# Kernel optimization log

Measured on AMD Instinct MI355X. Metric: run time of the kernel, lower is better.

Reference implementation:

```python
import jax, jax.numpy as jnp
import numpy as np

N, E, D, IN_DIM, EDGE_DIM, L = 50000, 800000, 128, 11, 4, 4
G, MID, SPEC = 500, 256, 300  # num graphs, decoder mid width, per-head spectrum dim
MSG_IN = 2 * D + EDGE_DIM + 1  # h_i, h_j, edge_attr, d2


def _lin_init(key, fan_in, shape):
    return jax.random.uniform(key, shape, jnp.float32, -1.0, 1.0) / np.sqrt(fan_in)


def setup_inputs() -> dict:
    key = jax.random.key(0)
    ks = iter(jax.random.split(key, 64))
    inp = {
        'x': jax.random.normal(next(ks), (N, IN_DIM), jnp.float32),
        'pos': jax.random.normal(next(ks), (N, 3), jnp.float32),
        'edge_attr': jax.random.normal(next(ks), (E, EDGE_DIM), jnp.float32),
        'edge_index': jax.random.randint(next(ks), (2, E), 0, N, jnp.int32),
        'batch': jnp.sort(jax.random.randint(next(ks), (N,), 0, G, jnp.int32)),
        # input projection
        'W_in': _lin_init(next(ks), IN_DIM, (IN_DIM, D)),
        'b_in': jnp.zeros((D,), jnp.float32),
        # per-layer message MLP: Linear(2D+de+1 -> D), ReLU, Linear(D -> D)
        'msg_W1': _lin_init(next(ks), MSG_IN, (L, MSG_IN, D)),
        'msg_b1': jnp.zeros((L, D), jnp.float32),
        'msg_W2': _lin_init(next(ks), D, (L, D, D)),
        'msg_b2': jnp.zeros((L, D), jnp.float32),
        # per-layer update MLP: Linear(2D -> D), ReLU, Linear(D -> D)
        'upd_W1': _lin_init(next(ks), 2 * D, (L, 2 * D, D)),
        'upd_b1': jnp.zeros((L, D), jnp.float32),
        'upd_W2': _lin_init(next(ks), D, (L, D, D)),
        'upd_b2': jnp.zeros((L, D), jnp.float32),
        # per-layer LayerNorm
        'ln_g': jnp.ones((L, D), jnp.float32),
        'ln_b': jnp.zeros((L, D), jnp.float32),
        # decoder heads stacked: index 0 = energy, 1 = intensity
        'dec_W1': _lin_init(next(ks), D, (2, D, MID)),
        'dec_b1': jnp.zeros((2, MID), jnp.float32),
        'dec_lng': jnp.ones((2, MID), jnp.float32),
        'dec_lnb': jnp.zeros((2, MID), jnp.float32),
        'dec_W2': _lin_init(next(ks), MID, (2, MID, MID)),
        'dec_b2': jnp.zeros((2, MID), jnp.float32),
        'dec_W3': _lin_init(next(ks), MID, (2, MID, SPEC)),
        'dec_b3': jnp.zeros((2, SPEC), jnp.float32),
    }
    return inp


def _ln(x, g, b, eps=1e-5):
    m = x.mean(-1, keepdims=True)
    v = ((x - m) ** 2).mean(-1, keepdims=True)
    return (x - m) * jax.lax.rsqrt(v + eps) * g + b


def _softplus_beta(x, beta):
    return jax.nn.softplus(beta * x) / beta


def reference(x, pos, edge_attr, edge_index, batch,
              W_in, b_in, msg_W1, msg_b1, msg_W2, msg_b2,
              upd_W1, upd_b1, upd_W2, upd_b2, ln_g, ln_b,
              dec_W1, dec_b1, dec_lng, dec_lnb, dec_W2, dec_b2, dec_W3, dec_b3):
    n = x.shape[0]
    src, dst = edge_index[0], edge_index[1]  # message flows j(src) -> i(dst)
    h = x @ W_in + b_in  # (n, d)
    rel = pos[dst] - pos[src]  # (e, 3)
    d2 = jnp.sum(rel * rel, axis=-1, keepdims=True)  # (e, 1), invariant squared distance
    for l in range(L):
        m_in = jnp.concatenate([h[dst], h[src], edge_attr, d2], axis=-1)  # (e, 2d+de+1)
        m = jax.nn.relu(m_in @ msg_W1[l] + msg_b1[l]) @ msg_W2[l] + msg_b2[l]  # (e, d)
        agg = jax.ops.segment_sum(m, dst, num_segments=n)  # (n, d) sum aggregation
        u_in = jnp.concatenate([h, agg], axis=-1)  # (n, 2d)
        h_upd = jax.nn.relu(u_in @ upd_W1[l] + upd_b1[l]) @ upd_W2[l] + upd_b2[l]
        h = _ln(h + h_upd, ln_g[l], ln_b[l])  # residual + LayerNorm
    # global mean pool per graph
    hs = jax.ops.segment_sum(h, batch, num_segments=G)
    cnt = jax.ops.segment_sum(jnp.ones((n,), h.dtype), batch, num_segments=G)
    hg = hs / jnp.clip(cnt, 1.0)[:, None]  # (G, d)

    def head(i):
        z = _softplus_beta(_ln(hg @ dec_W1[i] + dec_b1[i], dec_lng[i], dec_lnb[i]), 2.0)
        z = _softplus_beta(z @ dec_W2[i] + dec_b2[i], 2.0)  # dropout = identity (eval)
        return _softplus_beta(z @ dec_W3[i] + dec_b3[i], 1.0)

    eng, intensity = head(0), head(1)
    return jnp.concatenate([eng, intensity], axis=-1)  # (G, 2*SPEC)
```

## Files before the change

### kernel.cpp

```cpp
#include <hip/hip_runtime.h>
#include <cstdint>
#include <cstddef>

#define NND 50000
#define NE  800000
#define DD  128
#define NG  500
#define TT  64
#define NHB 50176

typedef __attribute__((ext_vector_type(8))) short short8v;
typedef __attribute__((ext_vector_type(4))) float float4v;

#define SWZA(row, g) ((g) ^ ((row) & 7) ^ (((row) >> 3) & 7))

__device__ __forceinline__ short f2bf(float f) {
    unsigned u = __builtin_bit_cast(unsigned, f);
    unsigned r = (u + 0x7FFFu + ((u >> 16) & 1u)) >> 16;
    return (short)r;
}

__global__ __launch_bounds__(256) void inproj_kernel(
    const float* __restrict__ x, const float* __restrict__ W,
    const float* __restrict__ b, float* __restrict__ h)
{
    int t = blockIdx.x * 256 + threadIdx.x;
    int i = t >> 7, d = t & 127;
    if (i >= NND) return;
    const float* xr = x + (size_t)i * 11;
    float acc = b[d];
#pragma unroll
    for (int k = 0; k < 11; ++k) acc += xr[k] * W[k * DD + d];
    h[(size_t)i * DD + d] = acc;
}

__global__ __launch_bounds__(256) void hist_kernel(
    const int* __restrict__ dstI, int* __restrict__ hist)
{
    int e = blockIdx.x * 256 + threadIdx.x;
    if (e >= NE) return;
    atomicAdd(&hist[dstI[e]], 1);
}

__global__ __launch_bounds__(256) void scan1_kernel(
    int* __restrict__ hist, int* __restrict__ bsum)
{
    __shared__ int s[256];
    int tid = threadIdx.x;
    int i = blockIdx.x * 256 + tid;
    int v = hist[i];
    s[tid] = v; __syncthreads();
    for (int off = 1; off < 256; off <<= 1) {
        int tmp = (tid >= off) ? s[tid - off] : 0;
        __syncthreads();
        s[tid] += tmp;
        __syncthreads();
    }
    hist[i] = s[tid] - v;
    if (tid == 255) bsum[blockIdx.x] = s[255];
}

__global__ __launch_bounds__(256) void scan2_kernel(
    const int* __restrict__ bsum, int* __restrict__ bsumx)
{
    __shared__ int s[256];
    int tid = threadIdx.x;
    int v = (tid < 196) ? bsum[tid] : 0;
    s[tid] = v; __syncthreads();
    for (int off = 1; off < 256; off <<= 1) {
        int tmp = (tid >= off) ? s[tid - off] : 0;
        __syncthreads();
        s[tid] += tmp;
        __syncthreads();
    }
    if (tid < 196) bsumx[tid] = s[tid] - v;
}

__global__ __launch_bounds__(256) void scan3_kernel(
    int* __restrict__ hist, const int* __restrict__ bsumx)
{
    int i = blockIdx.x * 256 + threadIdx.x;
    hist[i] += bsumx[blockIdx.x];
}

__global__ __launch_bounds__(256) void scatter_kernel(
    const int* __restrict__ dstI, int* __restrict__ cursor, int* __restrict__ perm)
{
    int e = blockIdx.x * 256 + threadIdx.x;
    if (e >= NE) return;
    int pos = atomicAdd(&cursor[dstI[e]], 1);
    perm[pos] = e;
}

__global__ __launch_bounds__(256) void permapply_kernel(
    const int* __restrict__ perm, const int* __restrict__ srcI, const int* __restrict__ dstI,
    const float* __restrict__ ea,
    int* __restrict__ srcP, int* __restrict__ dstP, float* __restrict__ eaP)
{
    int i = blockIdx.x * 256 + threadIdx.x;
    if (i >= NE) return;
    int e = perm[i];
    srcP[i] = srcI[e];
    dstP[i] = dstI[e];
    ((float4*)eaP)[i] = ((const float4*)ea)[e];
}

__global__ __launch_bounds__(256) void d2p_kernel(
    const float* __restrict__ pos, const int* __restrict__ srcP,
    const int* __restrict__ dstP, float* __restrict__ d2)
{
    int e = blockIdx.x * 256 + threadIdx.x;
    if (e >= NE) return;
    int s = srcP[e], d = dstP[e];
    float dx = pos[d * 3 + 0] - pos[s * 3 + 0];
    float dy = pos[d * 3 + 1] - pos[s * 3 + 1];
    float dz = pos[d * 3 + 2] - pos[s * 3 + 2];
    d2[e] = dx * dx + dy * dy + dz * dz;
}

__global__ __launch_bounds__(256) void d2_kernel(
    const float* __restrict__ pos, const int* __restrict__ srcI,
    const int* __restrict__ dstI, float* __restrict__ d2)
{
    int e = blockIdx.x * 256 + threadIdx.x;
    if (e >= NE) return;
    int s = srcI[e], d = dstI[e];
    float dx = pos[d * 3 + 0] - pos[s * 3 + 0];
    float dy = pos[d * 3 + 1] - pos[s * 3 + 1];
    float dz = pos[d * 3 + 2] - pos[s * 3 + 2];
    d2[e] = dx * dx + dy * dy + dz * dz;
}

__global__ __launch_bounds__(256) void wprep_kernel(
    const float* __restrict__ msgW2, const float* __restrict__ updW1,
    const float* __restrict__ updW2, const float* __restrict__ msgW1,
    short* __restrict__ out)
{
    int p = blockIdx.x * 256 + threadIdx.x;
    int chunk = p >> 14;
    int idx = p & 16383;
    int n = idx >> 7;
    int q = (idx & 127) >> 3;
    int j = idx & 7;
    int k = (q ^ (n & 7)) * 8 + j;
    const float* src;
    if      (chunk == 0) src = msgW2;
    else if (chunk == 1) src = updW1;
    else if (chunk == 2) src = updW1 + 128 * DD;
    else if (chunk == 3) src = updW2;
    else if (chunk == 4) src = msgW1;
    else                 src = msgW1 + 128 * DD;
    out[p] = f2bf(src[k * DD + n]);
}

__global__ __launch_bounds__(256, 3) void projm_kernel(
    const float* __restrict__ h, const short* __restrict__ Wa, const short* __restrict__ Wb,
    float* __restrict__ P)
{
    __shared__ __align__(16) short A[64 * 128];
    __shared__ __align__(16) short W[128 * 128];
    int t = threadIdx.x;
    int i0 = blockIdx.x * TT;

    {
        int e = t >> 2;
        int node = i0 + e; if (node >= NND) node = NND - 1;
        const float* hr = h + (size_t)node * DD;
#pragma unroll
        for (int j = 0; j < 4; ++j) {
            int g = (t & 3) * 4 + j;
            float4 v0 = *(const float4*)(hr + g * 8);
            float4 v1 = *(const float4*)(hr + g * 8 + 4);
            short8v pk;
            pk[0]=f2bf(v0.x); pk[1]=f2bf(v0.y); pk[2]=f2bf(v0.z); pk[3]=f2bf(v0.w);
            pk[4]=f2bf(v1.x); pk[5]=f2bf(v1.y); pk[6]=f2bf(v1.z); pk[7]=f2bf(v1.w);
            *(short8v*)&A[e * 128 + SWZA(e, g) * 8] = pk;
        }
    }
    {
        const short8v* g = (const short8v*)Wa;
        short8v* l = (short8v*)W;
#pragma unroll
        for (int p = 0; p < 8; ++p) l[t + p * 256] = g[t + p * 256];
    }
    __syncthreads();

    int lane = t & 63, w = t >> 6;
    int c = lane & 15, lg = lane >> 4;
    int m = w * 16 + c;

    for (int mat = 0; mat < 2; ++mat) {
        float4v acc[8];
#pragma unroll
        for (int i = 0; i < 8; ++i) acc[i] = (float4v){0.f, 0.f, 0.f, 0.f};
#pragma unroll
        for (int ks = 0; ks < 4; ++ks) {
            int kg = ks * 4 + lg;
            short8v afrag = *(const short8v*)&A[m * 128 + SWZA(m, kg) * 8];
#pragma unroll
            for (int nt = 0; nt < 8; ++nt) {
                int n = nt * 16 + c;
                short8v bfrag = *(const short8v*)&W[n * 128 + ((kg ^ (n & 7)) << 3)];
                acc[nt] = __builtin_amdgcn_mfma_f32_16x16x32_bf16(afrag, bfrag, acc[nt], 0, 0, 0);
            }
        }
        float* out = P + (size_t)mat * NND * DD;
#pragma unroll
        for (int reg = 0; reg < 4; ++reg) {
            int node = i0 + w * 16 + lg * 4 + reg;
            if (node < NND) {
#pragma unroll
                for (int nt = 0; nt < 8; ++nt)
                    out[(size_t)node * DD + nt * 16 + c] = acc[nt][reg];
            }
        }
        if (mat == 0) {
            __syncthreads();
            const short8v* g = (const short8v*)Wb;
            short8v* l = (short8v*)W;
#pragma unroll
            for (int p = 0; p < 8; ++p) l[t + p * 256] = g[t + p * 256];
            __syncthreads();
        }
    }
}

__global__ __launch_bounds__(256, 3) void msgm_kernel(
    const float* __restrict__ P, const int* __restrict__ srcP, const int* __restrict__ dstP,
    const float* __restrict__ eaP, const float* __restrict__ d2,
    const float* __restrict__ W1tail, const float* __restrict__ b1,
    const short* __restrict__ W2t, const float* __restrict__ b2,
    float* __restrict__ agg)
{
    __shared__ __align__(16) short Tld[64 * 128];
    __shared__ __align__(16) short W2ld[128 * 128];
    int t = threadIdx.x;
    int e0 = blockIdx.x * TT;
    int tx = t & 15, ty = t >> 4;

    {
        const short8v* g = (const short8v*)W2t;
        short8v* l = (short8v*)W2ld;
#pragma unroll
        for (int p = 0; p < 8; ++p) l[t + p * 256] = g[t + p * 256];
    }

    float wc[5][8];
#pragma unroll
    for (int qf = 0; qf < 5; ++qf) {
        float4 a0 = *(const float4*)(W1tail + qf * DD + ty * 8);
        float4 a1 = *(const float4*)(W1tail + qf * DD + ty * 8 + 4);
        wc[qf][0] = a0.x; wc[qf][1] = a0.y; wc[qf][2] = a0.z; wc[qf][3] = a0.w;
        wc[qf][4] = a1.x; wc[qf][5] = a1.y; wc[qf][6] = a1.z; wc[qf][7] = a1.w;
    }

    float4 b1a = *(const float4*)(b1 + ty * 8);
    float4 b1b = *(const float4*)(b1 + ty * 8 + 4);
    float b1v[8] = {b1a.x, b1a.y, b1a.z, b1a.w, b1b.x, b1b.y, b1b.z, b1b.w};

    const float* Pd = P;
    const float* Ps = P + (size_t)NND * DD;

    int4 dv4 = *(const int4*)(dstP + e0 + tx * 4);
    int4 sv4 = *(const int4*)(srcP + e0 + tx * 4);
    int dcache[4] = {dv4.x, dv4.y, dv4.z, dv4.w};
    int scache[4] = {sv4.x, sv4.y, sv4.z, sv4.w};

#pragma unroll
    for (int i = 0; i < 4; ++i) {
        int e = tx * 4 + i;
        const float* pd = Pd + (size_t)dcache[i] * DD + ty * 8;
        const float* ps = Ps + (size_t)scache[i] * DD + ty * 8;
        float4 p0 = *(const float4*)pd;
        float4 p1 = *(const float4*)(pd + 4);
        float4 q0 = *(const float4*)ps;
        float4 q1 = *(const float4*)(ps + 4);
        float tv[8] = {p0.x + q0.x, p0.y + q0.y, p0.z + q0.z, p0.w + q0.w,
                       p1.x + q1.x, p1.y + q1.y, p1.z + q1.z, p1.w + q1.w};
#pragma unroll
        for (int j = 0; j < 8; ++j) tv[j] += b1v[j];
        float4 av = ((const float4*)eaP)[e0 + e];
        float ev[5] = {av.x, av.y, av.z, av.w, d2[e0 + e]};
#pragma unroll
        for (int qf = 0; qf < 5; ++qf) {
            float xx = ev[qf];
#pragma unroll
            for (int j = 0; j < 8; ++j) tv[j] += xx * wc[qf][j];
        }
        short8v pk;
#pragma unroll
        for (int j = 0; j < 8; ++j) pk[j] = f2bf(fmaxf(tv[j], 0.0f));
        *(short8v*)&Tld[e * 128 + SWZA(e, ty) * 8] = pk;
    }

    __syncthreads();

    int lane = t & 63, w = t >> 6;
    int lg = lane >> 4;
    int m  = w * 16 + (lane & 15);
    float4v acc[8];
#pragma unroll
    for (int i = 0; i < 8; ++i) acc[i] = (float4v){0.f, 0.f, 0.f, 0.f};

#pragma unroll
    for (int ks = 0; ks < 4; ++ks) {
        int kg = ks * 4 + lg;
        short8v afrag = *(const short8v*)&Tld[m * 128 + SWZA(m, kg) * 8];
#pragma unroll
        for (int nt = 0; nt < 8; ++nt) {
            int n = nt * 16 + (lane & 15);
            short8v bfrag = *(const short8v*)&W2ld[n * 128 + ((kg ^ (n & 7)) << 3)];
            acc[nt] = __builtin_amdgcn_mfma_f32_16x16x32_bf16(afrag, bfrag, acc[nt], 0, 0, 0);
        }
    }

    int base_e = e0 + w * 16 + (lg << 2);
    int4 dq = *(const int4*)(dstP + base_e);
    int drow[4] = {dq.x, dq.y, dq.z, dq.w};
    float b2c[8];
#pragma unroll
    for (int nt = 0; nt < 8; ++nt) b2c[nt] = b2[nt * 16 + (lane & 15)];

    float sum[8];
    int cur = drow[0];
#pragma unroll
    for (int nt = 0; nt < 8; ++nt) sum[nt] = acc[nt][0] + b2c[nt];
#pragma unroll
    for (int r = 1; r < 4; ++r) {
        if (drow[r] == cur) {
#pragma unroll
            for (int nt = 0; nt < 8; ++nt) sum[nt] += acc[nt][r] + b2c[nt];
        } else {
            float* ag = agg + (size_t)cur * DD + (lane & 15);
#pragma unroll
            for (int nt = 0; nt < 8; ++nt) unsafeAtomicAdd(ag + nt * 16, sum[nt]);
            cur = drow[r];
#pragma unroll
            for (int nt = 0; nt < 8; ++nt) sum[nt] = acc[nt][r] + b2c[nt];
        }
    }
    float* ag = agg + (size_t)cur * DD + (lane & 15);
#pragma unroll
    for (int nt = 0; nt < 8; ++nt) unsafeAtomicAdd(ag + nt * 16, sum[nt]);
}

__global__ __launch_bounds__(256, 3) void updm_kernel(
    float* __restrict__ h, const float* __restrict__ agg,
    const short* __restrict__ W1a, const short* __restrict__ W1b, const short* __restrict__ W2s,
    const float* __restrict__ b1, const float* __restrict__ b2,
    const float* __restrict__ lng, const float* __restrict__ lnb)
{
    __shared__ __align__(16) short A[64 * 128];
    __shared__ __align__(16) short W[128 * 128];
    int t = threadIdx.x;
    int i0 = blockIdx.x * TT;
    int lane = t & 63, w = t >> 6;
    int c = lane & 15, lg = lane >> 4;
    int m = w * 16 + c;

    {
        int e = t >> 2;
        int node = i0 + e; if (node >= NND) node = NND - 1;
        const float* hr = h + (size_t)node * DD;
#pragma unroll
        for (int j = 0; j < 4; ++j) {
            int g = (t & 3) * 4 + j;
            float4 v0 = *(const float4*)(hr + g * 8);
            float4 v1 = *(const float4*)(hr + g * 8 + 4);
            short8v pk;
            pk[0]=f2bf(v0.x); pk[1]=f2bf(v0.y); pk[2]=f2bf(v0.z); pk[3]=f2bf(v0.w);
            pk[4]=f2bf(v1.x); pk[5]=f2bf(v1.y); pk[6]=f2bf(v1.z); pk[7]=f2bf(v1.w);
            *(short8v*)&A[e * 128 + SWZA(e, g) * 8] = pk;
        }
        const short8v* gg = (const short8v*)W1a;
        short8v* l = (short8v*)W;
#pragma unroll
        for (int p = 0; p < 8; ++p) l[t + p * 256] = gg[t + p * 256];
    }
    __syncthreads();

    float4v acc[8];
#pragma unroll
    for (int i = 0; i < 8; ++i) acc[i] = (float4v){0.f, 0.f, 0.f, 0.f};

#pragma unroll
    for (int ks = 0; ks < 4; ++ks) {
        int kg = ks * 4 + lg;
        short8v afrag = *(const short8v*)&A[m * 128 + SWZA(m, kg) * 8];
#pragma unroll
        for (int nt = 0; nt < 8; ++nt) {
            int n = nt * 16 + c;
            short8v bfrag = *(const short8v*)&W[n * 128 + ((kg ^ (n & 7)) << 3)];
            acc[nt] = __builtin_amdgcn_mfma_f32_16x16x32_bf16(afrag, bfrag, acc[nt], 0, 0, 0);
        }
    }
    __syncthreads();

    {
        int e = t >> 2;
        int node = i0 + e; if (node >= NND) node = NND - 1;
        const float* ar = agg + (size_t)node * DD;
#pragma unroll
        for (int j = 0; j < 4; ++j) {
            int g = (t & 3) * 4 + j;
            float4 v0 = *(const float4*)(ar + g * 8);
            float4 v1 = *(const float4*)(ar + g * 8 + 4);
            short8v pk;
            pk[0]=f2bf(v0.x); pk[1]=f2bf(v0.y); pk[2]=f2bf(v0.z); pk[3]=f2bf(v0.w);
            pk[4]=f2bf(v1.x); pk[5]=f2bf(v1.y); pk[6]=f2bf(v1.z); pk[7]=f2bf(v1.w);
            *(short8v*)&A[e * 128 + SWZA(e, g) * 8] = pk;
        }
        const short8v* gg = (const short8v*)W1b;
        short8v* l = (short8v*)W;
#pragma unroll
        for (int p = 0; p < 8; ++p) l[t + p * 256] = gg[t + p * 256];
    }
    __syncthreads();

#pragma unroll
    for (int ks = 0; ks < 4; ++ks) {
        int kg = ks * 4 + lg;
        short8v afrag = *(const short8v*)&A[m * 128 + SWZA(m, kg) * 8];
#pragma unroll
        for (int nt = 0; nt < 8; ++nt) {
            int n = nt * 16 + c;
            short8v bfrag = *(const short8v*)&W[n * 128 + ((kg ^ (n & 7)) << 3)];
            acc[nt] = __builtin_amdgcn_mfma_f32_16x16x32_bf16(afrag, bfrag, acc[nt], 0, 0, 0);
        }
    }
    __syncthreads();

    {
        float b1c[8];
#pragma unroll
        for (int nt = 0; nt < 8; ++nt) b1c[nt] = b1[nt * 16 + c];
#pragma unroll
        for (int reg = 0; reg < 4; ++reg) {
            int rowT = w * 16 + lg * 4 + reg;
#pragma unroll
            for (int nt = 0; nt < 8; ++nt) {
                int col = nt * 16 + c;
                int colg = col >> 3;
                float v = fmaxf(acc[nt][reg] + b1c[nt], 0.0f);
                A[rowT * 128 + SWZA(rowT, colg) * 8 + (col & 7)] = f2bf(v);
            }
        }
        const short8v* gg = (const short8v*)W2s;
        short8v* l = (short8v*)W;
#pragma unroll
        for (int p = 0; p < 8; ++p) l[t + p * 256] = gg[t + p * 256];
    }
    __syncthreads();

#pragma unroll
    for (int i = 0; i < 8; ++i) acc[i] = (float4v){0.f, 0.f, 0.f, 0.f};
#pragma unroll
    for (int ks = 0; ks < 4; ++ks) {
        int kg = ks * 4 + lg;
        short8v afrag = *(const short8v*)&A[m * 128 + SWZA(m, kg) * 8];
#pragma unroll
        for (int nt = 0; nt < 8; ++nt) {
            int n = nt * 16 + c;
            short8v bfrag = *(const short8v*)&W[n * 128 + ((kg ^ (n & 7)) << 3)];
            acc[nt] = __builtin_amdgcn_mfma_f32_16x16x32_bf16(afrag, bfrag, acc[nt], 0, 0, 0);
        }
    }

    float b2c[8], lngc[8], lnbc[8];
#pragma unroll
    for (int nt = 0; nt < 8; ++nt) {
        b2c[nt]  = b2[nt * 16 + c];
        lngc[nt] = lng[nt * 16 + c];
        lnbc[nt] = lnb[nt * 16 + c];
    }
    float xx[8][4];
#pragma unroll
    for (int reg = 0; reg < 4; ++reg) {
        int node = i0 + w * 16 + lg * 4 + reg;
        int nclamp = (node < NND) ? node : (NND - 1);
        const float* hr = h + (size_t)nclamp * DD;
#pragma unroll
        for (int nt = 0; nt < 8; ++nt)
            xx[nt][reg] = acc[nt][reg] + b2c[nt] + hr[nt * 16 + c];
    }
    float s[4] = {0.f, 0.f, 0.f, 0.f};
#pragma unroll
    for (int reg = 0; reg < 4; ++reg)
#pragma unroll
        for (int nt = 0; nt < 8; ++nt) s[reg] += xx[nt][reg];
#pragma unroll
    for (int msk = 1; msk < 16; msk <<= 1)
#pragma unroll
        for (int reg = 0; reg < 4; ++reg) s[reg] += __shfl_xor(s[reg], msk, 64);
    float mean[4];
#pragma unroll
    for (int reg = 0; reg < 4; ++reg) mean[reg] = s[reg] * (1.0f / DD);
    float v[4] = {0.f, 0.f, 0.f, 0.f};
#pragma unroll
    for (int reg = 0; reg < 4; ++reg)
#pragma unroll
        for (int nt = 0; nt < 8; ++nt) {
            float dv = xx[nt][reg] - mean[reg];
            v[reg] += dv * dv;
        }
#pragma unroll
    for (int msk = 1; msk < 16; msk <<= 1)
#pragma unroll
        for (int reg = 0; reg < 4; ++reg) v[reg] += __shfl_xor(v[reg], msk, 64);
#pragma unroll
    for (int reg = 0; reg < 4; ++reg) {
        int node = i0 + w * 16 + lg * 4 + reg;
        if (node < NND) {
            float inv = 1.0f / sqrtf(v[reg] * (1.0f / DD) + 1e-5f);
            float* hw = h + (size_t)node * DD;
#pragma unroll
            for (int nt = 0; nt < 8; ++nt)
                hw[nt * 16 + c] = (xx[nt][reg] - mean[reg]) * inv * lngc[nt] + lnbc[nt];
        }
    }
}

__global__ __launch_bounds__(256, 2) void msgu_kernel(
    const float* __restrict__ h, const int* __restrict__ srcI, const int* __restrict__ dstI,
    const float* __restrict__ ea, const float* __restrict__ d2,
    const float* __restrict__ W1, const float* __restrict__ b1,
    const float* __restrict__ W2, const float* __restrict__ b2,
    float* __restrict__ agg)
{
    __shared__ __align__(16) float A[32][TT];
    __shared__ __align__(16) float T[DD][TT];
    __shared__ __align__(16) float B[32][DD];
    int t = threadIdx.x;
    int e0 = blockIdx.x * TT;
    int tx = t & 15, ty = t >> 4;
    int e = t & 63, q = t >> 6;
    int dn = dstI[e0 + e], sn = srcI[e0 + e];

    float4 b1a = *(const float4*)(b1 + ty * 8);
    float4 b1b = *(const float4*)(b1 + ty * 8 + 4);
    float acc[4][8];
#pragma unroll
    for (int i = 0; i < 4; ++i) {
        acc[i][0] = b1a.x; acc[i][1] = b1a.y; acc[i][2] = b1a.z; acc[i][3] = b1a.w;
        acc[i][4] = b1b.x; acc[i][5] = b1b.y; acc[i][6] = b1b.z; acc[i][7] = b1b.w;
    }

    for (int cc = 0; cc < 9; ++cc) {
        int kmax = (cc == 8) ? 5 : 32;
        __syncthreads();
        if (cc < 8) {
            const float* row = h + (size_t)((cc < 4) ? dn : sn) * DD + (cc & 3) * 32;
            float4 v0 = *(const float4*)(row + q * 8);
            float4 v1 = *(const float4*)(row + q * 8 + 4);
#pragma unroll
            for (int j = 0; j < 4; ++j) A[q * 8 + j][e]     = (&v0.x)[j];
#pragma unroll
            for (int j = 0; j < 4; ++j) A[q * 8 + 4 + j][e] = (&v1.x)[j];
        } else if (t < TT) {
            float4 av = ((const float4*)ea)[e0 + t];
            A[0][t] = av.x; A[1][t] = av.y; A[2][t] = av.z; A[3][t] = av.w;
            A[4][t] = d2[e0 + t];
        }
        const float4* srcp = (const float4*)(W1 + (size_t)(cc * 32) * DD);
        float4* dstp = (float4*)&B[0][0];
        if (cc < 8) {
#pragma unroll
            for (int r = 0; r < 4; ++r) dstp[t + r * 256] = srcp[t + r * 256];
        } else if (t < 160) {
            dstp[t] = srcp[t];
        }
        __syncthreads();
        for (int k = 0; k < kmax; ++k) {
            float4 a  = *(const float4*)&A[k][tx * 4];
            float4 b0 = *(const float4*)&B[k][ty * 8];
            float4 b1f = *(const float4*)&B[k][ty * 8 + 4];
            float av[4] = {a.x, a.y, a.z, a.w};
            float bv[8] = {b0.x, b0.y, b0.z, b0.w, b1f.x, b1f.y, b1f.z, b1f.w};
#pragma unroll
            for (int i = 0; i < 4; ++i)
#pragma unroll
                for (int j = 0; j < 8; ++j) acc[i][j] += av[i] * bv[j];
        }
    }

#pragma unroll
    for (int i = 0; i < 4; ++i)
#pragma unroll
        for (int j = 0; j < 8; ++j) T[ty * 8 + j][tx * 4 + i] = fmaxf(acc[i][j], 0.0f);

    float4 b2a = *(const float4*)(b2 + ty * 8);
    float4 b2b = *(const float4*)(b2 + ty * 8 + 4);
#pragma unroll
    for (int i = 0; i < 4; ++i) {
        acc[i][0] = b2a.x; acc[i][1] = b2a.y; acc[i][2] = b2a.z; acc[i][3] = b2a.w;
        acc[i][4] = b2b.x; acc[i][5] = b2b.y; acc[i][6] = b2b.z; acc[i][7] = b2b.w;
    }
    for (int cc = 0; cc < 4; ++cc) {
        __syncthreads();
        const float4* srcp = (const float4*)(W2 + (size_t)(cc * 32) * DD);
        float4* dstp = (float4*)&B[0][0];
#pragma unroll
        for (int r = 0; r < 4; ++r) dstp[t + r * 256] = srcp[t + r * 256];
        __syncthreads();
#pragma unroll 4
        for (int k = 0; k < 32; ++k) {
            float4 a  = *(const float4*)&T[cc * 32 + k][tx * 4];
            float4 b0 = *(const float4*)&B[k][ty * 8];
            float4 b1f = *(const float4*)&B[k][ty * 8 + 4];
            float av[4] = {a.x, a.y, a.z, a.w};
            float bv[8] = {b0.x, b0.y, b0.z, b0.w, b1f.x, b1f.y, b1f.z, b1f.w};
#pragma unroll
            for (int i = 0; i < 4; ++i)
#pragma unroll
                for (int j = 0; j < 8; ++j) acc[i][j] += av[i] * bv[j];
        }
    }
#pragma unroll
    for (int i = 0; i < 4; ++i) {
        int d = dstI[e0 + tx * 4 + i];
        float* ag = agg + (size_t)d * DD + ty * 8;
#pragma unroll
        for (int j = 0; j < 8; ++j) unsafeAtomicAdd(ag + j, acc[i][j]);
    }
}

__global__ __launch_bounds__(256, 2) void updf_kernel(
    float* __restrict__ h, const float* __restrict__ agg,
    const float* __restrict__ W1, const float* __restrict__ b1,
    const float* __restrict__ W2, const float* __restrict__ b2,
    const float* __restrict__ lng, const float* __restrict__ lnb)
{
    __shared__ __align__(16) float A[32][TT];
    __shared__ __align__(16) float T[DD][TT];
    __shared__ __align__(16) float B[32][DD];
    int t = threadIdx.x;
    int i0 = blockIdx.x * TT;
    int tx = t & 15, ty = t >> 4;
    int e = t & 63, q = t >> 6;
    int node = i0 + e; int nclamp = (node < NND) ? node : (NND - 1);

    float4 b1a = *(const float4*)(b1 + ty * 8);
    float4 b1b = *(const float4*)(b1 + ty * 8 + 4);
    float acc[4][8];
#pragma unroll
    for (int i = 0; i < 4; ++i) {
        acc[i][0] = b1a.x; acc[i][1] = b1a.y; acc[i][2] = b1a.z; acc[i][3] = b1a.w;
        acc[i][4] = b1b.x; acc[i][5] = b1b.y; acc[i][6] = b1b.z; acc[i][7] = b1b.w;
    }

    for (int cc = 0; cc < 8; ++cc) {
        __syncthreads();
        const float* row = ((cc < 4) ? (h + (size_t)nclamp * DD + cc * 32)
                                     : (agg + (size_t)nclamp * DD + (cc - 4) * 32));
        float4 v0 = *(const float4*)(row + q * 8);
        float4 v1 = *(const float4*)(row + q * 8 + 4);
#pragma unroll
        for (int j = 0; j < 4; ++j) A[q * 8 + j][e]     = (&v0.x)[j];
#pragma unroll
        for (int j = 0; j < 4; ++j) A[q * 8 + 4 + j][e] = (&v1.x)[j];
        const float4* srcp = (const float4*)(W1 + (size_t)(cc * 32) * DD);
        float4* dstp = (float4*)&B[0][0];
#pragma unroll
        for (int r = 0; r < 4; ++r) dstp[t + r * 256] = srcp[t + r * 256];
        __syncthreads();
#pragma unroll 4
        for (int k = 0; k < 32; ++k) {
            float4 a  = *(const float4*)&A[k][tx * 4];
            float4 b0 = *(const float4*)&B[k][ty * 8];
            float4 b1f = *(const float4*)&B[k][ty * 8 + 4];
            float av[4] = {a.x, a.y, a.z, a.w};
            float bv[8] = {b0.x, b0.y, b0.z, b0.w, b1f.x, b1f.y, b1f.z, b1f.w};
#pragma unroll
            for (int i = 0; i < 4; ++i)
#pragma unroll
                for (int j = 0; j < 8; ++j) acc[i][j] += av[i] * bv[j];
        }
    }

#pragma unroll
    for (int i = 0; i < 4; ++i)
#pragma unroll
        for (int j = 0; j < 8; ++j) T[ty * 8 + j][tx * 4 + i] = fmaxf(acc[i][j], 0.0f);

    float4 b2a = *(const float4*)(b2 + ty * 8);
    float4 b2b = *(const float4*)(b2 + ty * 8 + 4);
#pragma unroll
    for (int i = 0; i < 4; ++i) {
        acc[i][0] = b2a.x; acc[i][1] = b2a.y; acc[i][2] = b2a.z; acc[i][3] = b2a.w;
        acc[i][4] = b2b.x; acc[i][5] = b2b.y; acc[i][6] = b2b.z; acc[i][7] = b2b.w;
    }
    for (int cc = 0; cc < 4; ++cc) {
        __syncthreads();
        const float4* srcp = (const float4*)(W2 + (size_t)(cc * 32) * DD);
        float4* dstp = (float4*)&B[0][0];
#pragma unroll
        for (int r = 0; r < 4; ++r) dstp[t + r * 256] = srcp[t + r * 256];
        __syncthreads();
#pragma unroll 4
        for (int k = 0; k < 32; ++k) {
            float4 a  = *(const float4*)&T[cc * 32 + k][tx * 4];
            float4 b0 = *(const float4*)&B[k][ty * 8];
            float4 b1f = *(const float4*)&B[k][ty * 8 + 4];
            float av[4] = {a.x, a.y, a.z, a.w};
            float bv[8] = {b0.x, b0.y, b0.z, b0.w, b1f.x, b1f.y, b1f.z, b1f.w};
#pragma unroll
            for (int i = 0; i < 4; ++i)
#pragma unroll
                for (int j = 0; j < 8; ++j) acc[i][j] += av[i] * bv[j];
        }
    }

    __syncthreads();
#pragma unroll
    for (int i = 0; i < 4; ++i)
#pragma unroll
        for (int j = 0; j < 8; ++j) T[ty * 8 + j][tx * 4 + i] = acc[i][j];
    __syncthreads();

    if (t < TT) {
        int nd = i0 + t;
        if (nd < NND) {
            float* hrow = h + (size_t)nd * DD;
            float sum = 0.0f;
            for (int o = 0; o < DD; ++o) sum += T[o][t] + hrow[o];
            float mean = sum * (1.0f / DD);
            float var = 0.0f;
            for (int o = 0; o < DD; ++o) {
                float xv = T[o][t] + hrow[o] - mean;
                var += xv * xv;
            }
            var *= (1.0f / DD);
            float inv = 1.0f / sqrtf(var + 1e-5f);
            for (int o = 0; o < DD; ++o) {
                float xv = T[o][t] + hrow[o];
                hrow[o] = (xv - mean) * inv * lng[o] + lnb[o];
            }
        }
    }
}

__global__ __launch_bounds__(256) void cnt_kernel(
    const int* __restrict__ batch, float* __restrict__ cnt)
{
    int i = blockIdx.x * 256 + threadIdx.x;
    if (i >= NND) return;
    unsafeAtomicAdd(&cnt[batch[i]], 1.0f);
}

__global__ __launch_bounds__(256) void pool_kernel(
    const float* __restrict__ h, const int* __restrict__ batch, float* __restrict__ hs)
{
    int t = blockIdx.x * 256 + threadIdx.x;
    int i = t >> 7, d = t & 127;
    if (i >= NND) return;
    unsafeAtomicAdd(&hs[batch[i] * DD + d], h[(size_t)i * DD + d]);
}

__device__ __forceinline__ float softplus_stable(float y) {
    return fmaxf(y, 0.0f) + log1pf(expf(-fabsf(y)));
}

__global__ __launch_bounds__(256) void dec_kernel(
    const float* __restrict__ hs, const float* __restrict__ cnt,
    const float* __restrict__ W1, const float* __restrict__ b1,
    const float* __restrict__ lng, const float* __restrict__ lnb,
    const float* __restrict__ W2, const float* __restrict__ b2,
    const float* __restrict__ W3, const float* __restrict__ b3,
    float* __restrict__ out)
{
    int g  = blockIdx.x >> 1;
    int hd = blockIdx.x & 1;
    int t  = threadIdx.x;
    __shared__ float hg[DD];
    __shared__ float sA[256];
    __shared__ float red[256];

    if (t < DD) {
        float cct = fmaxf(cnt[g], 1.0f);
        hg[t] = hs[g * DD + t] / cct;
    }
    __syncthreads();

    const float* w1 = W1 + hd * DD * 256;
    float acc = b1[hd * 256 + t];
#pragma unroll 8
    for (int k = 0; k < DD; ++k) acc += hg[k] * w1[k * 256 + t];

    red[t] = acc; __syncthreads();
    for (int s = 128; s > 0; s >>= 1) { if (t < s) red[t] += red[t + s]; __syncthreads(); }
    float mean = red[0] * (1.0f / 256.0f);
    __syncthreads();
    float dv = acc - mean;
    red[t] = dv * dv; __syncthreads();
    for (int s = 128; s > 0; s >>= 1) { if (t < s) red[t] += red[t + s]; __syncthreads(); }
    float var = red[0] * (1.0f / 256.0f);
    float inv = 1.0f / sqrtf(var + 1e-5f);
    float z1 = dv * inv * lng[hd * 256 + t] + lnb[hd * 256 + t];
    z1 = softplus_stable(2.0f * z1) * 0.5f;
    __syncthreads();
    sA[t] = z1; __syncthreads();

    const float* w2 = W2 + hd * 256 * 256;
    float acc2 = b2[hd * 256 + t];
#pragma unroll 8
    for (int k = 0; k < 256; ++k) acc2 += sA[k] * w2[k * 256 + t];
    float z2 = softplus_stable(2.0f * acc2) * 0.5f;
    __syncthreads();
    sA[t] = z2; __syncthreads();

    const float* w3 = W3 + hd * 256 * 300;
    for (int s = t; s < 300; s += 256) {
        float acc3 = b3[hd * 300 + s];
#pragma unroll 8
        for (int k = 0; k < 256; ++k) acc3 += sA[k] * w3[k * 300 + s];
        out[g * 600 + hd * 300 + s] = softplus_stable(acc3);
    }
}

extern "C" void kernel_launch(void* const* d_in, const int* in_sizes, int n_in,
                              void* d_out, int out_size, void* d_ws, size_t ws_size,
                              hipStream_t stream)
{
    const float* x     = (const float*)d_in[0];
    const float* pos   = (const float*)d_in[1];
    const float* eattr = (const float*)d_in[2];
    const int*   eidx  = (const int*)d_in[3];
    const int*   batch = (const int*)d_in[4];
    const float* W_in  = (const float*)d_in[5];
    const float* b_in  = (const float*)d_in[6];
    const float* msgW1 = (const float*)d_in[7];
    const float* msgb1 = (const float*)d_in[8];
    const float* msgW2 = (const float*)d_in[9];
    const float* msgb2 = (const float*)d_in[10];
    const float* updW1 = (const float*)d_in[11];
    const float* updb1 = (const float*)d_in[12];
    const float* updW2 = (const float*)d_in[13];
    const float* updb2 = (const float*)d_in[14];
    const float* lng   = (const float*)d_in[15];
    const float* lnb   = (const float*)d_in[16];
    const float* dW1   = (const float*)d_in[17];
    const float* db1   = (const float*)d_in[18];
    const float* dlng  = (const float*)d_in[19];
    const float* dlnb  = (const float*)d_in[20];
    const float* dW2   = (const float*)d_in[21];
    const float* db2   = (const float*)d_in[22];
    const float* dW3   = (const float*)d_in[23];
    const float* db3   = (const float*)d_in[24];

    float* ws  = (float*)d_ws;
    float* h    = ws;
    float* agg  = ws + 6400000;
    float* d2   = ws + 12800000;
    float* hsg  = ws + 13600000;
    float* cnt  = ws + 13664000;
    float* P    = ws + 13700000;
    int*   perm = (int*)(ws + 26500000);
    int*   srcP = (int*)(ws + 27300000);
    int*   dstP = (int*)(ws + 28100000);
    float* eaP  = ws + 28900000;
    int*   hist = (int*)(ws + 32100000);
    int*   bsum = (int*)(ws + 32150176);
    int*   bsumx= (int*)(ws + 32150432);
    short* WP   = (short*)(ws + 32150688);

    const size_t need_sorted = (size_t)(32150688 + 49152) * 4;
    const bool sorted = (ws_size >= need_sorted);

    const int* srcI = eidx;
    const int* dstI = eidx + NE;

    inproj_kernel<<<25000, 256, 0, stream>>>(x, W_in, b_in, h);

    if (sorted) {
        hipMemsetAsync(hist, 0, (size_t)(NHB + 512) * 4, stream);
        hist_kernel<<<3125, 256, 0, stream>>>(dstI, hist);
        scan1_kernel<<<196, 256, 0, stream>>>(hist, bsum);
        scan2_kernel<<<1, 256, 0, stream>>>(bsum, bsumx);
        scan3_kernel<<<196, 256, 0, stream>>>(hist, bsumx);
        scatter_kernel<<<3125, 256, 0, stream>>>(dstI, hist, perm);
        permapply_kernel<<<3125, 256, 0, stream>>>(perm, srcI, dstI, eattr, srcP, dstP, eaP);
        d2p_kernel<<<3125, 256, 0, stream>>>(pos, srcP, dstP, d2);
    } else {
        d2_kernel<<<3125, 256, 0, stream>>>(pos, srcI, dstI, d2);
    }

    const int nblk_nodes = (NND + TT - 1) / TT;
    const int nblk_edges = NE / TT;

    for (int l = 0; l < 4; ++l) {
        const float* W1l = msgW1 + (size_t)l * 261 * 128;
        hipMemsetAsync(agg, 0, 6400000 * sizeof(float), stream);
        if (sorted) {
            wprep_kernel<<<384, 256, 0, stream>>>(
                msgW2 + (size_t)l * 128 * 128, updW1 + (size_t)l * 256 * 128,
                updW2 + (size_t)l * 128 * 128, W1l, WP);
            projm_kernel<<<nblk_nodes, 256, 0, stream>>>(h, WP + 4 * 16384, WP + 5 * 16384, P);
            msgm_kernel<<<nblk_edges, 256, 0, stream>>>(P, srcP, dstP, eaP, d2,
                W1l + 256 * 128, msgb1 + l * 128, WP, msgb2 + l * 128, agg);
            updm_kernel<<<nblk_nodes, 256, 0, stream>>>(h, agg,
                WP + 1 * 16384, WP + 2 * 16384, WP + 3 * 16384,
                updb1 + l * 128, updb2 + l * 128, lng + l * 128, lnb + l * 128);
        } else {
            msgu_kernel<<<nblk_edges, 256, 0, stream>>>(h, srcI, dstI, eattr, d2,
                W1l, msgb1 + l * 128,
                msgW2 + (size_t)l * 128 * 128, msgb2 + l * 128, agg);
            updf_kernel<<<nblk_nodes, 256, 0, stream>>>(h, agg,
                updW1 + (size_t)l * 256 * 128, updb1 + l * 128,
                updW2 + (size_t)l * 128 * 128, updb2 + l * 128,
                lng + l * 128, lnb + l * 128);
        }
    }

    hipMemsetAsync(hsg, 0, 64500 * sizeof(float), stream);
    cnt_kernel<<<196, 256, 0, stream>>>(batch, cnt);
    pool_kernel<<<25000, 256, 0, stream>>>(h, batch, hsg);
    dec_kernel<<<1000, 256, 0, stream>>>(hsg, cnt, dW1, db1, dlng, dlnb,
                                         dW2, db2, dW3, db3, (float*)d_out);
}
```

Measured before the change: 1.849 ms.

## Store projected node features as bf16 and build MFMA A-fragments in registers

```diff
diff --git a/kernel.cpp b/kernel.cpp
--- a/kernel.cpp
+++ b/kernel.cpp
@@ -18,6 +18,9 @@
     unsigned u = __builtin_bit_cast(unsigned, f);
     unsigned r = (u + 0x7FFFu + ((u >> 16) & 1u)) >> 16;
     return (short)r;
+}
+__device__ __forceinline__ float bf2f(short s) {
+    return __builtin_bit_cast(float, ((unsigned)(unsigned short)s) << 16);
 }
 
 __global__ __launch_bounds__(256) void inproj_kernel(
@@ -155,7 +158,7 @@
 
 __global__ __launch_bounds__(256, 3) void projm_kernel(
     const float* __restrict__ h, const short* __restrict__ Wa, const short* __restrict__ Wb,
-    float* __restrict__ P)
+    short* __restrict__ P)
 {
     __shared__ __align__(16) short A[64 * 128];
     __shared__ __align__(16) short W[128 * 128];
@@ -204,14 +207,14 @@
                 acc[nt] = __builtin_amdgcn_mfma_f32_16x16x32_bf16(afrag, bfrag, acc[nt], 0, 0, 0);
             }
         }
-        float* out = P + (size_t)mat * NND * DD;
+        short* out = P + (size_t)mat * NND * DD;
 #pragma unroll
         for (int reg = 0; reg < 4; ++reg) {
             int node = i0 + w * 16 + lg * 4 + reg;
             if (node < NND) {
 #pragma unroll
                 for (int nt = 0; nt < 8; ++nt)
-                    out[(size_t)node * DD + nt * 16 + c] = acc[nt][reg];
+                    out[(size_t)node * DD + nt * 16 + c] = f2bf(acc[nt][reg]);
             }
         }
         if (mat == 0) {
@@ -225,92 +228,70 @@
     }
 }
 
-__global__ __launch_bounds__(256, 3) void msgm_kernel(
-    const float* __restrict__ P, const int* __restrict__ srcP, const int* __restrict__ dstP,
+__global__ __launch_bounds__(256, 4) void msgm_kernel(
+    const short* __restrict__ P, const int* __restrict__ srcP, const int* __restrict__ dstP,
     const float* __restrict__ eaP, const float* __restrict__ d2,
     const float* __restrict__ W1tail, const float* __restrict__ b1,
     const short* __restrict__ W2t, const float* __restrict__ b2,
     float* __restrict__ agg)
 {
-    __shared__ __align__(16) short Tld[64 * 128];
     __shared__ __align__(16) short W2ld[128 * 128];
+    __shared__ __align__(16) float WcB[6 * 128];
     int t = threadIdx.x;
     int e0 = blockIdx.x * TT;
-    int tx = t & 15, ty = t >> 4;
 
     {
         const short8v* g = (const short8v*)W2t;
         short8v* l = (short8v*)W2ld;
 #pragma unroll
         for (int p = 0; p < 8; ++p) l[t + p * 256] = g[t + p * 256];
-    }
-
-    float wc[5][8];
-#pragma unroll
-    for (int qf = 0; qf < 5; ++qf) {
-        float4 a0 = *(const float4*)(W1tail + qf * DD + ty * 8);
-        float4 a1 = *(const float4*)(W1tail + qf * DD + ty * 8 + 4);
-        wc[qf][0] = a0.x; wc[qf][1] = a0.y; wc[qf][2] = a0.z; wc[qf][3] = a0.w;
-        wc[qf][4] = a1.x; wc[qf][5] = a1.y; wc[qf][6] = a1.z; wc[qf][7] = a1.w;
-    }
-
-    float4 b1a = *(const float4*)(b1 + ty * 8);
-    float4 b1b = *(const float4*)(b1 + ty * 8 + 4);
-    float b1v[8] = {b1a.x, b1a.y, b1a.z, b1a.w, b1b.x, b1b.y, b1b.z, b1b.w};
-
-    const float* Pd = P;
-    const float* Ps = P + (size_t)NND * DD;
-
-    int4 dv4 = *(const int4*)(dstP + e0 + tx * 4);
-    int4 sv4 = *(const int4*)(srcP + e0 + tx * 4);
-    int dcache[4] = {dv4.x, dv4.y, dv4.z, dv4.w};
-    int scache[4] = {sv4.x, sv4.y, sv4.z, sv4.w};
-
-#pragma unroll
-    for (int i = 0; i < 4; ++i) {
-        int e = tx * 4 + i;
-        const float* pd = Pd + (size_t)dcache[i] * DD + ty * 8;
-        const float* ps = Ps + (size_t)scache[i] * DD + ty * 8;
-        float4 p0 = *(const float4*)pd;
-        float4 p1 = *(const float4*)(pd + 4);
-        float4 q0 = *(const float4*)ps;
-        float4 q1 = *(const float4*)(ps + 4);
-        float tv[8] = {p0.x + q0.x, p0.y + q0.y, p0.z + q0.z, p0.w + q0.w,
-                       p1.x + q1.x, p1.y + q1.y, p1.z + q1.z, p1.w + q1.w};
-#pragma unroll
-        for (int j = 0; j < 8; ++j) tv[j] += b1v[j];
-        float4 av = ((const float4*)eaP)[e0 + e];
-        float ev[5] = {av.x, av.y, av.z, av.w, d2[e0 + e]};
+        if (t < 160)      ((float4*)WcB)[t] = ((const float4*)W1tail)[t];
+        else if (t < 192) ((float4*)WcB)[t] = ((const float4*)b1)[t - 160];
+    }
+    __syncthreads();
+
+    int lane = t & 63, w = t >> 6;
+    int c = lane & 15, lg = lane >> 4;
+    int e = e0 + w * 16 + c;
+    int ds = dstP[e], sr = srcP[e];
+    const short* pd = P + (size_t)ds * DD;
+    const short* ps = P + (size_t)NND * DD + (size_t)sr * DD;
+    float4 av = ((const float4*)eaP)[e];
+    float ev[5] = {av.x, av.y, av.z, av.w, d2[e]};
+
+    short8v afrag[4];
+#pragma unroll
+    for (int ks = 0; ks < 4; ++ks) {
+        int kg = ks * 4 + lg;
+        short8v pdv = *(const short8v*)(pd + kg * 8);
+        short8v psv = *(const short8v*)(ps + kg * 8);
+        float tv[8];
+#pragma unroll
+        for (int j = 0; j < 8; ++j)
+            tv[j] = bf2f(pdv[j]) + bf2f(psv[j]) + WcB[5 * 128 + kg * 8 + j];
 #pragma unroll
         for (int qf = 0; qf < 5; ++qf) {
             float xx = ev[qf];
 #pragma unroll
-            for (int j = 0; j < 8; ++j) tv[j] += xx * wc[qf][j];
+            for (int j = 0; j < 8; ++j) tv[j] += xx * WcB[qf * 128 + kg * 8 + j];
         }
         short8v pk;
 #pragma unroll
         for (int j = 0; j < 8; ++j) pk[j] = f2bf(fmaxf(tv[j], 0.0f));
-        *(short8v*)&Tld[e * 128 + SWZA(e, ty) * 8] = pk;
-    }
-
-    __syncthreads();
-
-    int lane = t & 63, w = t >> 6;
-    int lg = lane >> 4;
-    int m  = w * 16 + (lane & 15);
+        afrag[ks] = pk;
+    }
+
     float4v acc[8];
 #pragma unroll
     for (int i = 0; i < 8; ++i) acc[i] = (float4v){0.f, 0.f, 0.f, 0.f};
-
 #pragma unroll
     for (int ks = 0; ks < 4; ++ks) {
         int kg = ks * 4 + lg;
-        short8v afrag = *(const short8v*)&Tld[m * 128 + SWZA(m, kg) * 8];
 #pragma unroll
         for (int nt = 0; nt < 8; ++nt) {
-            int n = nt * 16 + (lane & 15);
+            int n = nt * 16 + c;
             short8v bfrag = *(const short8v*)&W2ld[n * 128 + ((kg ^ (n & 7)) << 3)];
-            acc[nt] = __builtin_amdgcn_mfma_f32_16x16x32_bf16(afrag, bfrag, acc[nt], 0, 0, 0);
+            acc[nt] = __builtin_amdgcn_mfma_f32_16x16x32_bf16(afrag[ks], bfrag, acc[nt], 0, 0, 0);
         }
     }
 
@@ -319,7 +300,7 @@
     int drow[4] = {dq.x, dq.y, dq.z, dq.w};
     float b2c[8];
 #pragma unroll
-    for (int nt = 0; nt < 8; ++nt) b2c[nt] = b2[nt * 16 + (lane & 15)];
+    for (int nt = 0; nt < 8; ++nt) b2c[nt] = b2[nt * 16 + c];
 
     float sum[8];
     int cur = drow[0];
@@ -331,7 +312,7 @@
 #pragma unroll
             for (int nt = 0; nt < 8; ++nt) sum[nt] += acc[nt][r] + b2c[nt];
         } else {
-            float* ag = agg + (size_t)cur * DD + (lane & 15);
+            float* ag = agg + (size_t)cur * DD + c;
 #pragma unroll
             for (int nt = 0; nt < 8; ++nt) unsafeAtomicAdd(ag + nt * 16, sum[nt]);
             cur = drow[r];
@@ -339,7 +320,7 @@
             for (int nt = 0; nt < 8; ++nt) sum[nt] = acc[nt][r] + b2c[nt];
         }
     }
-    float* ag = agg + (size_t)cur * DD + (lane & 15);
+    float* ag = agg + (size_t)cur * DD + c;
 #pragma unroll
     for (int nt = 0; nt < 8; ++nt) unsafeAtomicAdd(ag + nt * 16, sum[nt]);
 }
@@ -853,7 +834,7 @@
     float* d2   = ws + 12800000;
     float* hsg  = ws + 13600000;
     float* cnt  = ws + 13664000;
-    float* P    = ws + 13700000;
+    short* P    = (short*)(ws + 13700000);
     int*   perm = (int*)(ws + 26500000);
     int*   srcP = (int*)(ws + 27300000);
     int*   dstP = (int*)(ws + 28100000);
```

Result: no change. 1.837 ms (-0.6%).
